# Kernel tuning notes

Hardware: AMD Instinct MI355X
Metric: run time of the kernel (lower is better)

Reference implementation:

```python
import jax, jax.numpy as jnp
import numpy as np

N = 100000
F_IN = 128
E = 1_600_000
NEG_SLOPE = 0.2  # PyG GATConv default negative_slope


def _seg_sum(v, idx, n):
    return jax.ops.segment_sum(v, idx, num_segments=n)


def gcn_conv(x, W, b, src, dst, n):
    # PyG GCNConv: D^{-1/2} (A + I) D^{-1/2} X W + b (self loops already in src/dst)
    h = x @ W
    deg = _seg_sum(jnp.ones(src.shape, h.dtype), dst, n)
    dinv = jnp.where(deg > 0, jax.lax.rsqrt(deg), 0.0)
    norm = dinv[src] * dinv[dst]  # [E]
    return _seg_sum(h[src] * norm[:, None], dst, n) + b


def gat_conv(x, W, a_src, a_dst, b, src, dst, n, heads, out_ch):
    # PyG GATConv (concat=True), eval mode (dropout inactive)
    h = (x @ W).reshape(n, heads, out_ch)          # [n,H,C]
    s = jnp.einsum('nhc,hc->nh', h, a_src)          # per-node src score
    t = jnp.einsum('nhc,hc->nh', h, a_dst)          # per-node dst score
    e = jax.nn.leaky_relu(s[src] + t[dst], NEG_SLOPE)  # [E,H]
    m = jax.ops.segment_max(e, dst, num_segments=n)    # stable segment softmax
    m = jnp.where(jnp.isfinite(m), m, 0.0)
    p = jnp.exp(e - m[dst])
    denom = _seg_sum(p, dst, n)
    alpha = p / (denom[dst] + 1e-16)                 # [E,H]
    out = _seg_sum(h[src] * alpha[:, :, None], dst, n)  # [n,H,C]
    return out.reshape(n, heads * out_ch) + b


def setup_inputs():
    key = jax.random.key(0)
    ks = jax.random.split(key, 24)
    x = jax.random.normal(ks[0], (N, F_IN), jnp.float32) * 0.1
    half = N // 2
    # one-hot user/item type flags read by forward (x[:,0]==1 / x[:,1]==1)
    x = x.at[:, 0].set(0.0).at[:, 1].set(0.0)
    x = x.at[:half, 0].set(1.0).at[half:, 1].set(1.0)
    src = jax.random.randint(ks[1], (E,), 0, N, dtype=jnp.int32)
    dst = jax.random.randint(ks[2], (E,), 0, N, dtype=jnp.int32)
    edge_index = jnp.stack([src, dst])

    def p(k, shape):
        return jax.random.normal(k, shape, jnp.float32) * 0.1

    inp = {"x": x, "edge_index": edge_index,
           "gcn_w": p(ks[3], (F_IN, 16)), "gcn_b": jnp.zeros((16,), jnp.float32)}
    dims = [(16, 16, 8), (128, 16, 8), (128, 16, 8), (128, 2, 1)]
    for i, (fi, fo, h) in enumerate(dims, start=1):
        inp[f"g{i}_w"] = p(ks[3 + 4 * i], (fi, h * fo))
        inp[f"g{i}_as"] = p(ks[4 + 4 * i], (h, fo))
        inp[f"g{i}_ad"] = p(ks[5 + 4 * i], (h, fo))
        inp[f"g{i}_b"] = jnp.zeros((h * fo,), jnp.float32)
    return inp


def reference(x, edge_index, gcn_w, gcn_b,
              g1_w, g1_as, g1_ad, g1_b,
              g2_w, g2_as, g2_ad, g2_b,
              g3_w, g3_as, g3_ad, g3_b,
              g4_w, g4_as, g4_ad, g4_b):
    n = x.shape[0]
    loops = jnp.arange(n, dtype=edge_index.dtype)  # self loops (added by GCN/GAT layers)
    src = jnp.concatenate([edge_index[0], loops])
    dst = jnp.concatenate([edge_index[1], loops])
    h = jax.nn.elu(gcn_conv(x, gcn_w, gcn_b, src, dst, n))
    h = jax.nn.elu(gat_conv(h, g1_w, g1_as, g1_ad, g1_b, src, dst, n, 8, 16))
    h = jax.nn.elu(gat_conv(h, g2_w, g2_as, g2_ad, g2_b, src, dst, n, 8, 16))
    h = jax.nn.elu(gat_conv(h, g3_w, g3_as, g3_ad, g3_b, src, dst, n, 8, 16))
    h = jax.nn.elu(gat_conv(h, g4_w, g4_as, g4_ad, g4_b, src, dst, n, 1, 2))  # [n,2]
    half = n // 2  # users are rows [:half], items rows [half:]
    out = jnp.concatenate([h[:half], h[half:]], axis=1)  # [half,4]
    return jax.nn.log_softmax(out, axis=1)
```

## Files before the change

### kernel.cpp

```cpp
#include <hip/hip_runtime.h>
#include <cstddef>
#include <cstdint>

#define NN 100000
#define NPAD 100032
#define NE 1600000
#define ET (NE + NN)
#define ETP_MAX (ET + 8 * NN)
#define HALFN (NN / 2)
#define NEG_SLOPE 0.2f
#define SCB 1024
#define DMAX 96
#define RP 8
#define RNODES (NN / RP)
#define CHUNK 8192

typedef __attribute__((ext_vector_type(8))) short short8v;
typedef __attribute__((ext_vector_type(4))) float float4v;
typedef __attribute__((ext_vector_type(2))) float float2v;

__device__ __forceinline__ float lrelu(float x) { return x > 0.f ? x : NEG_SLOPE * x; }

__device__ __forceinline__ uint16_t f2bf(float f) {
  uint32_t u = __float_as_uint(f);
  uint32_t r = u + 0x7fffu + ((u >> 16) & 1u);
  return (uint16_t)(r >> 16);
}
__device__ __forceinline__ float bflo(uint32_t u) { return __uint_as_float(u << 16); }
__device__ __forceinline__ float bfhi(uint32_t u) { return __uint_as_float(u & 0xffff0000u); }

template<int K, int M>
__launch_bounds__(256)
__global__ void gemm4_kernel(const float* __restrict__ X, const float* __restrict__ W,
                             float* __restrict__ Y, int n) {
  constexpr int CG = M / 4;
  constexpr int RG = 256 / CG;
  constexpr int RPT = 2;
  constexpr int RT = RG * RPT;
  constexpr int KP = K + 1;
  __shared__ __align__(16) float sW[K * M];
  __shared__ float sX[RT * KP];
  for (int i = threadIdx.x; i < K * M; i += 256) sW[i] = W[i];
  const int jg = threadIdx.x % CG;
  const int rg = threadIdx.x / CG;
  const int r0 = rg * RPT;
  for (int base = blockIdx.x * RT; base < n; base += gridDim.x * RT) {
    __syncthreads();
    const int nrows = (n - base) < RT ? (n - base) : RT;
    for (int i = threadIdx.x; i < nrows * K; i += 256) {
      int r = i / K, c = i - r * K;
      sX[r * KP + c] = X[(size_t)base * K + i];
    }
    __syncthreads();
    float acc[RPT][4];
    #pragma unroll
    for (int rr = 0; rr < RPT; ++rr) acc[rr][0] = acc[rr][1] = acc[rr][2] = acc[rr][3] = 0.f;
    #pragma unroll 4
    for (int k = 0; k < K; ++k) {
      const float4 w = *(const float4*)&sW[k * M + jg * 4];
      #pragma unroll
      for (int rr = 0; rr < RPT; ++rr) {
        const float xv = sX[(r0 + rr) * KP + k];
        acc[rr][0] = fmaf(xv, w.x, acc[rr][0]);
        acc[rr][1] = fmaf(xv, w.y, acc[rr][1]);
        acc[rr][2] = fmaf(xv, w.z, acc[rr][2]);
        acc[rr][3] = fmaf(xv, w.w, acc[rr][3]);
      }
    }
    #pragma unroll
    for (int rr = 0; rr < RPT; ++rr) {
      if (r0 + rr < nrows) {
        float4 o = make_float4(acc[rr][0], acc[rr][1], acc[rr][2], acc[rr][3]);
        *(float4*)&Y[(size_t)(base + r0 + rr) * M + jg * 4] = o;
      }
    }
  }
}

template<int KB>
__launch_bounds__(256)
__global__ void wpack_kernel(const float* __restrict__ W, uint16_t* __restrict__ wp,
                             int Kreal) {
  int tid = blockIdx.x * 256 + threadIdx.x;
  if (tid >= KB * 8 * 64) return;
  int lane = tid & 63;
  int ctkb = tid >> 6;
  int kb = ctkb % KB, ct = ctkb / KB;
  int nc = ct * 16 + (lane & 15);
  int k0 = kb * 32 + (lane >> 4) * 8;
  ushort4 o0, o1;
  uint16_t v[8];
  #pragma unroll
  for (int j = 0; j < 8; ++j) {
    int k = k0 + j;
    v[j] = (k < Kreal) ? f2bf(W[(size_t)k * 128 + nc]) : (uint16_t)0;
  }
  o0.x = v[0]; o0.y = v[1]; o0.z = v[2]; o0.w = v[3];
  o1.x = v[4]; o1.y = v[5]; o1.z = v[6]; o1.w = v[7];
  *(ushort4*)&wp[(size_t)tid * 8] = o0;
  *(ushort4*)&wp[(size_t)tid * 8 + 4] = o1;
}

template<int KB, int XS>
__launch_bounds__(256)
__global__ void gemm_mfma_kernel(const uint16_t* __restrict__ X,
                                 const uint16_t* __restrict__ wp,
                                 uint16_t* __restrict__ Y, int n) {
  __shared__ float sC[4][16 * 136];
  const int wv = threadIdx.x >> 6;
  const int lane = threadIdx.x & 63;
  const int rowbase = blockIdx.x * 64 + wv * 16;
  int arow = rowbase + (lane & 15);
  if (arow >= n) arow = n - 1;
  const uint16_t* xp = X + (size_t)arow * XS + ((lane >> 4) * 8);
  short8v a[KB];
  #pragma unroll
  for (int kb = 0; kb < KB; ++kb) a[kb] = *(const short8v*)(xp + kb * 32);
  #pragma unroll
  for (int ct = 0; ct < 8; ++ct) {
    float4v acc = {0.f, 0.f, 0.f, 0.f};
    #pragma unroll
    for (int kb = 0; kb < KB; ++kb) {
      short8v b = *(const short8v*)&wp[(size_t)((ct * KB + kb) * 64 + lane) * 8];
      acc = __builtin_amdgcn_mfma_f32_16x16x32_bf16(a[kb], b, acc, 0, 0, 0);
    }
    #pragma unroll
    for (int r = 0; r < 4; ++r)
      sC[wv][((lane >> 4) * 4 + r) * 136 + ct * 16 + (lane & 15)] = acc[r];
  }
  #pragma unroll
  for (int t = 0; t < 4; ++t) {
    int idx = t * 64 + lane;
    int row = idx >> 4;
    int c8 = idx & 15;
    const float* pr = &sC[wv][row * 136 + c8 * 8];
    float4 lo = *(const float4*)pr;
    float4 hi = *(const float4*)(pr + 4);
    uint4 o;
    o.x = (uint32_t)f2bf(lo.x) | ((uint32_t)f2bf(lo.y) << 16);
    o.y = (uint32_t)f2bf(lo.z) | ((uint32_t)f2bf(lo.w) << 16);
    o.z = (uint32_t)f2bf(hi.x) | ((uint32_t)f2bf(hi.y) << 16);
    o.w = (uint32_t)f2bf(hi.z) | ((uint32_t)f2bf(hi.w) << 16);
    *(uint4*)&Y[(size_t)(rowbase + row) * 128 + c8 * 8] = o;
  }
}

template<int K, int M, int ROWS>
__launch_bounds__(256)
__global__ void gemm_s_kernel(const uint16_t* __restrict__ Xb, const float* __restrict__ W,
                              float* __restrict__ Y, int n) {
  constexpr int KP = K + 1;
  __shared__ float sW[K * M];
  __shared__ float sX[ROWS * KP];
  for (int i = threadIdx.x; i < K * M; i += 256) sW[i] = W[i];
  for (int base = blockIdx.x * ROWS; base < n; base += gridDim.x * ROWS) {
    __syncthreads();
    const int nrows = (n - base) < ROWS ? (n - base) : ROWS;
    for (int i = threadIdx.x; i < nrows * (K / 4); i += 256) {
      int r = i / (K / 4), c = i - r * (K / 4);
      uint2 u = *(const uint2*)&Xb[(size_t)(base + r) * K + c * 4];
      sX[r * KP + c * 4 + 0] = bflo(u.x);
      sX[r * KP + c * 4 + 1] = bfhi(u.x);
      sX[r * KP + c * 4 + 2] = bflo(u.y);
      sX[r * KP + c * 4 + 3] = bfhi(u.y);
    }
    __syncthreads();
    for (int o = threadIdx.x; o < nrows * M; o += 256) {
      int r = o / M, j = o - r * M;
      float a = 0.f;
      #pragma unroll
      for (int k = 0; k < K; ++k) a = fmaf(sX[r * KP + k], sW[k * M + j], a);
      Y[(size_t)(base + r) * M + j] = a;
    }
  }
}

template<int H, int C>
__launch_bounds__(256)
__global__ void score_bf16_kernel(const uint32_t* __restrict__ Hm,
                                  const float* __restrict__ aS, const float* __restrict__ aD,
                                  float* __restrict__ S, float* __restrict__ T, int n) {
  int idx = blockIdx.x * 256 + threadIdx.x;
  int tot = n * H;
  if (idx >= tot + H) return;
  if (idx >= tot) { S[idx] = -1e30f; T[idx] = 0.f; return; }
  int h = idx & (H - 1);
  const uint32_t* hp = Hm + (size_t)idx * (C / 2);
  float s = 0.f, t = 0.f;
  #pragma unroll
  for (int c2 = 0; c2 < C / 2; ++c2) {
    uint32_t u = hp[c2];
    float v0 = bflo(u), v1 = bfhi(u);
    s = fmaf(v0, aS[h * C + 2 * c2], s);
    s = fmaf(v1, aS[h * C + 2 * c2 + 1], s);
    t = fmaf(v0, aD[h * C + 2 * c2], t);
    t = fmaf(v1, aD[h * C + 2 * c2 + 1], t);
  }
  S[idx] = s;
  T[idx] = t;
}

template<int H, int C>
__launch_bounds__(256)
__global__ void score_kernel(const float* __restrict__ Hm,
                             const float* __restrict__ aS, const float* __restrict__ aD,
                             float* __restrict__ S, float* __restrict__ T, int n) {
  int idx = blockIdx.x * 256 + threadIdx.x;
  int tot = n * H;
  if (idx >= tot + H) return;
  if (idx >= tot) { S[idx] = -1e30f; T[idx] = 0.f; return; }
  int h = idx & (H - 1);
  const float* hp = Hm + (size_t)idx * C;
  float s = 0.f, t = 0.f;
  #pragma unroll
  for (int c = 0; c < C; ++c) {
    float v = hp[c];
    s = fmaf(v, aS[h * C + c], s);
    t = fmaf(v, aD[h * C + c], t);
  }
  S[idx] = s;
  T[idx] = t;
}

__launch_bounds__(256)
__global__ void rank_kernel(const int* __restrict__ edst, int* __restrict__ cursor,
                            int* __restrict__ rank) {
  int e = blockIdx.x * 256 + threadIdx.x;
  if (e >= ET) return;
  int dn = e < NE ? edst[e] : e - NE;
  rank[e] = atomicAdd(&cursor[dn], 1);
}

__device__ __forceinline__ int pad8(int d) { return (d + 7) & ~7; }

__launch_bounds__(256)
__global__ void scan1_kernel(const int* __restrict__ degi, int* __restrict__ rowptr,
                             int* __restrict__ bsums) {
  __shared__ int sd[256];
  int t = threadIdx.x;
  int base = blockIdx.x * SCB + t * 4;
  int v0 = base + 0 < NN ? pad8(degi[base + 0]) : 0;
  int v1 = base + 1 < NN ? pad8(degi[base + 1]) : 0;
  int v2 = base + 2 < NN ? pad8(degi[base + 2]) : 0;
  int v3 = base + 3 < NN ? pad8(degi[base + 3]) : 0;
  int s = v0 + v1 + v2 + v3;
  sd[t] = s;
  __syncthreads();
  for (int off = 1; off < 256; off <<= 1) {
    int x = (t >= off) ? sd[t - off] : 0;
    __syncthreads();
    sd[t] += x;
    __syncthreads();
  }
  int excl = sd[t] - s;
  if (t == 255) bsums[blockIdx.x] = sd[255];
  if (base + 0 < NN) rowptr[base + 0] = excl;
  excl += v0;
  if (base + 1 < NN) rowptr[base + 1] = excl;
  excl += v1;
  if (base + 2 < NN) rowptr[base + 2] = excl;
  excl += v2;
  if (base + 3 < NN) rowptr[base + 3] = excl;
}

__launch_bounds__(256)
__global__ void scan2_kernel(int* __restrict__ bsums, int nb) {
  __shared__ int sd[256];
  int t = threadIdx.x;
  int v = t < nb ? bsums[t] : 0;
  sd[t] = v;
  __syncthreads();
  for (int off = 1; off < 256; off <<= 1) {
    int x = (t >= off) ? sd[t - off] : 0;
    __syncthreads();
    sd[t] += x;
    __syncthreads();
  }
  if (t < nb) bsums[t] = sd[t] - v;
  if (t == nb - 1) bsums[nb] = sd[t];
}

__launch_bounds__(256)
__global__ void scan3_kernel(int* __restrict__ rowptr, const int* __restrict__ bsums, int nb) {
  int i = blockIdx.x * 256 + threadIdx.x;
  if (i < NN) rowptr[i] += bsums[i / SCB];
  if (i == 0) rowptr[NN] = bsums[nb];
}

__launch_bounds__(256)
__global__ void dinv_kernel(const int* __restrict__ deg, float* __restrict__ dinv) {
  int i = blockIdx.x * 256 + threadIdx.x;
  if (i > NN) return;
  if (i == NN) { dinv[i] = 0.f; return; }
  int d = deg[i];
  dinv[i] = d > 0 ? rsqrtf((float)d) : 0.f;
}

__launch_bounds__(256)
__global__ void csr_fill_kernel(int* __restrict__ csr) {
  int i = blockIdx.x * 256 + threadIdx.x;
  if (i < ETP_MAX) csr[i] = NN;
}

__launch_bounds__(256)
__global__ void scatter_part_kernel(const int* __restrict__ esrc, const int* __restrict__ edst,
                                    const int* __restrict__ rowptr, const int* __restrict__ rank,
                                    int* __restrict__ csr_src) {
  int p = blockIdx.x & (RP - 1);
  int c = blockIdx.x >> 3;
  int lo = p * RNODES, hi = lo + RNODES;
  int e0 = c * CHUNK;
  int e1 = e0 + CHUNK < ET ? e0 + CHUNK : ET;
  for (int e = e0 + threadIdx.x; e < e1; e += 256) {
    int dn = e < NE ? edst[e] : e - NE;
    if (dn >= lo && dn < hi) {
      int sn = e < NE ? esrc[e] : e - NE;
      csr_src[rowptr[dn] + rank[e]] = sn;
    }
  }
}

__launch_bounds__(256)
__global__ void fused_gat_kernel(const int* __restrict__ rowptr, const int* __restrict__ csr,
                                 const float* __restrict__ S, const float* __restrict__ T,
                                 const uint16_t* __restrict__ Hm, const float* __restrict__ bias,
                                 float* __restrict__ galpha, uint16_t* __restrict__ Outb) {
  __shared__ float lds_p[4][DMAX * 9];
  __shared__ int   lds_c[4][DMAX];
  const int wv = threadIdx.x >> 6;
  const int lane = threadIdx.x & 63;
  const int d = (blockIdx.x * 256 + threadIdx.x) >> 6;
  if (d >= NN) return;
  const int rs = rowptr[d];
  const int deg = rowptr[d + 1] - rs;
  const int degL = deg < DMAX ? deg : DMAX;
  const char* sb = (const char*)S;
  const char* hb = (const char*)Hm;
  const int h = lane & 7, g = lane >> 3;
  const float Th = T[(size_t)d * 8 + h];
  float m = -1e30f;
  for (int l = g; l < degL; l += 8) {
    int sn = csr[rs + l];
    float sv = *(const float*)(sb + (((uint32_t)sn << 5) + (h << 2)));
    float e = lrelu(sv + Th);
    lds_p[wv][l * 9 + h] = e;
    if (h == 0) lds_c[wv][l] = sn;
    m = fmaxf(m, e);
  }
  for (int l = DMAX + g; l < deg; l += 8) {
    int sn = csr[rs + l];
    float e = lrelu(*(const float*)(sb + (((uint32_t)sn << 5) + (h << 2))) + Th);
    galpha[(size_t)(rs + l) * 8 + h] = e;
    m = fmaxf(m, e);
  }
  #pragma unroll
  for (int mask = 8; mask < 64; mask <<= 1) m = fmaxf(m, __shfl_xor(m, mask));
  float sum = 0.f;
  for (int l = g; l < degL; l += 8) {
    float p = __expf(lds_p[wv][l * 9 + h] - m);
    lds_p[wv][l * 9 + h] = p;
    sum += p;
  }
  for (int l = DMAX + g; l < deg; l += 8) {
    float p = __expf(galpha[(size_t)(rs + l) * 8 + h] - m);
    galpha[(size_t)(rs + l) * 8 + h] = p;
    sum += p;
  }
  #pragma unroll
  for (int mask = 8; mask < 64; mask <<= 1) sum += __shfl_xor(sum, mask);
  const float inv = 1.f / (sum + 1e-16f);
  const int eg = lane >> 4;
  const int cl = lane & 15;
  const int hp = cl >> 1;
  const float invp = __shfl(inv, hp);
  float2v A0 = {0.f, 0.f}, A1 = {0.f, 0.f}, A2 = {0.f, 0.f}, A3 = {0.f, 0.f};
  const uint32_t clo = (uint32_t)(cl << 4);
  #pragma unroll 2
  for (int l0 = 0; l0 < degL; l0 += 4) {
    int lc = l0 + eg;
    int sn = lds_c[wv][lc];
    float p = lds_p[wv][lc * 9 + hp];
    float2v pp = {p, p};
    uint4 u = *(const uint4*)(hb + (((uint32_t)sn << 8) + clo));
    float2v h0 = {bflo(u.x), bfhi(u.x)};
    float2v h1 = {bflo(u.y), bfhi(u.y)};
    float2v h2 = {bflo(u.z), bfhi(u.z)};
    float2v h3 = {bflo(u.w), bfhi(u.w)};
    A0 = pp * h0 + A0;
    A1 = pp * h1 + A1;
    A2 = pp * h2 + A2;
    A3 = pp * h3 + A3;
  }
  for (int l0 = DMAX; l0 < deg; l0 += 4) {
    int lc = l0 + eg;
    int sn = csr[rs + lc];
    float p = galpha[(size_t)(rs + lc) * 8 + hp];
    float2v pp = {p, p};
    uint4 u = *(const uint4*)(hb + (((uint32_t)sn << 8) + clo));
    float2v h0 = {bflo(u.x), bfhi(u.x)};
    float2v h1 = {bflo(u.y), bfhi(u.y)};
    float2v h2 = {bflo(u.z), bfhi(u.z)};
    float2v h3 = {bflo(u.w), bfhi(u.w)};
    A0 = pp * h0 + A0;
    A1 = pp * h1 + A1;
    A2 = pp * h2 + A2;
    A3 = pp * h3 + A3;
  }
  #pragma unroll
  for (int mask = 16; mask < 64; mask <<= 1) {
    A0.x += __shfl_xor(A0.x, mask); A0.y += __shfl_xor(A0.y, mask);
    A1.x += __shfl_xor(A1.x, mask); A1.y += __shfl_xor(A1.y, mask);
    A2.x += __shfl_xor(A2.x, mask); A2.y += __shfl_xor(A2.y, mask);
    A3.x += __shfl_xor(A3.x, mask); A3.y += __shfl_xor(A3.y, mask);
  }
  if (lane < 16) {
    float4 b0 = *(const float4*)&bias[cl * 8];
    float4 b1 = *(const float4*)&bias[cl * 8 + 4];
    float v0 = fmaf(A0.x, invp, b0.x), v1 = fmaf(A0.y, invp, b0.y);
    float v2 = fmaf(A1.x, invp, b0.z), v3 = fmaf(A1.y, invp, b0.w);
    float v4 = fmaf(A2.x, invp, b1.x), v5 = fmaf(A2.y, invp, b1.y);
    float v6 = fmaf(A3.x, invp, b1.z), v7 = fmaf(A3.y, invp, b1.w);
    v0 = v0 > 0.f ? v0 : expm1f(v0); v1 = v1 > 0.f ? v1 : expm1f(v1);
    v2 = v2 > 0.f ? v2 : expm1f(v2); v3 = v3 > 0.f ? v3 : expm1f(v3);
    v4 = v4 > 0.f ? v4 : expm1f(v4); v5 = v5 > 0.f ? v5 : expm1f(v5);
    v6 = v6 > 0.f ? v6 : expm1f(v6); v7 = v7 > 0.f ? v7 : expm1f(v7);
    uint4 o;
    o.x = (uint32_t)f2bf(v0) | ((uint32_t)f2bf(v1) << 16);
    o.y = (uint32_t)f2bf(v2) | ((uint32_t)f2bf(v3) << 16);
    o.z = (uint32_t)f2bf(v4) | ((uint32_t)f2bf(v5) << 16);
    o.w = (uint32_t)f2bf(v6) | ((uint32_t)f2bf(v7) << 16);
    *(uint4*)&Outb[(size_t)d * 128 + cl * 8] = o;
  }
}

__launch_bounds__(256)
__global__ void fused_gat1_kernel(const int* __restrict__ rowptr, const int* __restrict__ csr,
                                  const float* __restrict__ S, const float* __restrict__ T,
                                  const float* __restrict__ Hm2, const float* __restrict__ bias,
                                  float* __restrict__ galpha, float* __restrict__ Out) {
  int d = (blockIdx.x * 256 + threadIdx.x) >> 6;
  if (d >= NN) return;
  int lane = threadIdx.x & 63;
  int rs = rowptr[d], deg = rowptr[d + 1] - rs;
  float Td = T[d];
  int sn = 0;
  float e = -1e30f;
  if (lane < deg) { sn = csr[rs + lane]; e = lrelu(S[sn] + Td); }
  float m = e;
  for (int l2 = 64 + lane; l2 < deg; l2 += 64) {
    float e2 = lrelu(S[csr[rs + l2]] + Td);
    galpha[rs + l2] = e2;
    m = fmaxf(m, e2);
  }
  #pragma unroll
  for (int mask = 1; mask < 64; mask <<= 1) m = fmaxf(m, __shfl_xor(m, mask));
  float p = (lane < deg) ? __expf(e - m) : 0.f;
  float sum = p;
  for (int l2 = 64 + lane; l2 < deg; l2 += 64) {
    float p2 = __expf(galpha[rs + l2] - m);
    galpha[rs + l2] = p2;
    sum += p2;
  }
  #pragma unroll
  for (int mask = 1; mask < 64; mask <<= 1) sum += __shfl_xor(sum, mask);
  float inv = 1.f / (sum + 1e-16f);
  float a0 = 0.f, a1 = 0.f;
  if (lane < deg) {
    float2 hv = *(const float2*)&Hm2[(size_t)sn * 2];
    a0 = p * hv.x; a1 = p * hv.y;
  }
  for (int l2 = 64 + lane; l2 < deg; l2 += 64) {
    int sn2 = csr[rs + l2];
    float p2 = galpha[rs + l2];
    float2 hv = *(const float2*)&Hm2[(size_t)sn2 * 2];
    a0 = fmaf(p2, hv.x, a0); a1 = fmaf(p2, hv.y, a1);
  }
  #pragma unroll
  for (int mask = 1; mask < 64; mask <<= 1) {
    a0 += __shfl_xor(a0, mask); a1 += __shfl_xor(a1, mask);
  }
  if (lane == 0) {
    float v0 = fmaf(a0, inv, bias[0]);
    float v1 = fmaf(a1, inv, bias[1]);
    v0 = v0 > 0.f ? v0 : expm1f(v0);
    v1 = v1 > 0.f ? v1 : expm1f(v1);
    float2 o; o.x = v0; o.y = v1;
    *(float2*)&Out[(size_t)d * 2] = o;
  }
}

__launch_bounds__(256)
__global__ void gcn_pull_kernel(const int* __restrict__ rowptr, const int* __restrict__ csr_src,
                                const float* __restrict__ dinv, const float* __restrict__ Hm,
                                const float* __restrict__ bias, uint16_t* __restrict__ Outb) {
  int d = blockIdx.x * 16 + threadIdx.x / 16;
  if (d >= NN) return;
  int f = threadIdx.x & 15;
  int rs = rowptr[d], re = rowptr[d + 1];
  float acc = 0.f;
  int j = rs;
  for (; j + 4 <= re; j += 4) {
    int s0 = csr_src[j], s1 = csr_src[j + 1], s2 = csr_src[j + 2], s3 = csr_src[j + 3];
    float d0 = dinv[s0], d1 = dinv[s1], d2 = dinv[s2], d3 = dinv[s3];
    float h0 = Hm[(size_t)s0 * 16 + f], h1 = Hm[(size_t)s1 * 16 + f];
    float h2 = Hm[(size_t)s2 * 16 + f], h3 = Hm[(size_t)s3 * 16 + f];
    acc = fmaf(d0, h0, acc); acc = fmaf(d1, h1, acc);
    acc = fmaf(d2, h2, acc); acc = fmaf(d3, h3, acc);
  }
  for (; j < re; ++j) {
    int sn = csr_src[j];
    acc = fmaf(dinv[sn], Hm[(size_t)sn * 16 + f], acc);
  }
  float v = acc * dinv[d] + bias[f];
  v = v > 0.f ? v : expm1f(v);
  Outb[(size_t)d * 32 + f] = f2bf(v);
  Outb[(size_t)d * 32 + 16 + f] = 0;
}

__launch_bounds__(256)
__global__ void final_kernel(const float* __restrict__ A, float* __restrict__ Out) {
  int i = blockIdx.x * 256 + threadIdx.x;
  if (i >= HALFN) return;
  float v0 = A[(size_t)i * 2 + 0];
  float v1 = A[(size_t)i * 2 + 1];
  float v2 = A[(size_t)(i + HALFN) * 2 + 0];
  float v3 = A[(size_t)(i + HALFN) * 2 + 1];
  float m = fmaxf(fmaxf(v0, v1), fmaxf(v2, v3));
  float e0 = __expf(v0 - m), e1 = __expf(v1 - m), e2 = __expf(v2 - m), e3 = __expf(v3 - m);
  float l = logf(e0 + e1 + e2 + e3) + m;
  Out[(size_t)i * 4 + 0] = v0 - l;
  Out[(size_t)i * 4 + 1] = v1 - l;
  Out[(size_t)i * 4 + 2] = v2 - l;
  Out[(size_t)i * 4 + 3] = v3 - l;
}

extern "C" void kernel_launch(void* const* d_in, const int* in_sizes, int n_in,
                              void* d_out, int out_size, void* d_ws, size_t ws_size,
                              hipStream_t stream) {
  const float* x     = (const float*)d_in[0];
  const int*   eidx  = (const int*)d_in[1];
  const int*   esrc  = eidx;
  const int*   edst  = eidx + NE;
  const float* gcn_w = (const float*)d_in[2];
  const float* gcn_b = (const float*)d_in[3];

  char* ws = (char*)d_ws;
  uint16_t* hbf    = (uint16_t*)(ws + 0);
  uint16_t* bufAb  = (uint16_t*)(ws + 25700000);
  uint16_t* gcnHbf = (uint16_t*)(ws + 51400000);
  float*    bufB   = (float*)   (ws + 57900000);
  float*    bufC   = (float*)   (ws + 64400000);
  float*    Sb     = (float*)   (ws + 65300000);
  float*    Tb     = (float*)   (ws + 68600000);
  float*    galpha = (float*)   (ws + 71900000);
  int*      rowptr = (int*)     (ws + 151900000);
  int*      cursor = (int*)     (ws + 152300008);
  int*      csr    = (int*)     (ws + 152700008);
  float*    dinv   = (float*)   (ws + 162700008);
  int*      bsums  = (int*)     (ws + 163100016);
  int*      rank   = (int*)     (ws + 163100528);
  uint16_t* wpck   = (uint16_t*)(ws + 169900528);

  constexpr int NB_SCAN = (NN + SCB - 1) / SCB;

  hipMemsetAsync(cursor, 0, (size_t)NN * 4, stream);
  rank_kernel<<<(ET + 255) / 256, 256, 0, stream>>>(edst, cursor, rank);
  scan1_kernel<<<NB_SCAN, 256, 0, stream>>>(cursor, rowptr, bsums);
  scan2_kernel<<<1, 256, 0, stream>>>(bsums, NB_SCAN);
  scan3_kernel<<<(NN + 256) / 256, 256, 0, stream>>>(rowptr, bsums, NB_SCAN);
  dinv_kernel<<<(NN + 256) / 256, 256, 0, stream>>>(cursor, dinv);
  csr_fill_kernel<<<(ETP_MAX + 255) / 256, 256, 0, stream>>>(csr);
  {
    int nch = (ET + CHUNK - 1) / CHUNK;
    scatter_part_kernel<<<nch * RP, 256, 0, stream>>>(esrc, edst, rowptr, rank, csr);
  }

  {
    int tiles = (NN + 127) / 128;
    if (tiles > 4096) tiles = 4096;
    gemm4_kernel<128, 16><<<tiles, 256, 0, stream>>>(x, gcn_w, bufB, NN);
  }
  gcn_pull_kernel<<<(NN + 15) / 16, 256, 0, stream>>>(rowptr, csr, dinv, bufB, gcn_b, gcnHbf);

  wpack_kernel<1><<<2, 256, 0, stream>>>((const float*)d_in[4], wpck, 16);
  gemm_mfma_kernel<1, 32><<<NPAD / 64, 256, 0, stream>>>(gcnHbf, wpck, hbf, NN);
  score_bf16_kernel<8, 16><<<(NN * 8 + 8 + 255) / 256, 256, 0, stream>>>(
      (const uint32_t*)hbf, (const float*)d_in[5], (const float*)d_in[6], Sb, Tb, NN);
  fused_gat_kernel<<<(NN * 64 + 255) / 256, 256, 0, stream>>>(
      rowptr, csr, Sb, Tb, hbf, (const float*)d_in[7], galpha, bufAb);

  wpack_kernel<4><<<8, 256, 0, stream>>>((const float*)d_in[8], wpck, 128);
  gemm_mfma_kernel<4, 128><<<NPAD / 64, 256, 0, stream>>>(bufAb, wpck, hbf, NN);
  score_bf16_kernel<8, 16><<<(NN * 8 + 8 + 255) / 256, 256, 0, stream>>>(
      (const uint32_t*)hbf, (const float*)d_in[9], (const float*)d_in[10], Sb, Tb, NN);
  fused_gat_kernel<<<(NN * 64 + 255) / 256, 256, 0, stream>>>(
      rowptr, csr, Sb, Tb, hbf, (const float*)d_in[11], galpha, bufAb);

  wpack_kernel<4><<<8, 256, 0, stream>>>((const float*)d_in[12], wpck, 128);
  gemm_mfma_kernel<4, 128><<<NPAD / 64, 256, 0, stream>>>(bufAb, wpck, hbf, NN);
  score_bf16_kernel<8, 16><<<(NN * 8 + 8 + 255) / 256, 256, 0, stream>>>(
      (const uint32_t*)hbf, (const float*)d_in[13], (const float*)d_in[14], Sb, Tb, NN);
  fused_gat_kernel<<<(NN * 64 + 255) / 256, 256, 0, stream>>>(
      rowptr, csr, Sb, Tb, hbf, (const float*)d_in[15], galpha, bufAb);

  {
    int tiles = (NN + 127) / 128;
    if (tiles > 2048) tiles = 2048;
    gemm_s_kernel<128, 2, 128><<<tiles, 256, 0, stream>>>(
        bufAb, (const float*)d_in[16], bufB, NN);
    score_kernel<1, 2><<<(NN + 1 + 255) / 256, 256, 0, stream>>>(
        bufB, (const float*)d_in[17], (const float*)d_in[18], Sb, Tb, NN);
    fused_gat1_kernel<<<(NN * 64 + 255) / 256, 256, 0, stream>>>(
        rowptr, csr, Sb, Tb, bufB, (const float*)d_in[19], galpha, bufC);
  }

  final_kernel<<<(HALFN + 255) / 256, 256, 0, stream>>>(bufC, (float*)d_out);
}
```

Before: 585.4 us.

## Use single-pass online softmax in GAT aggregation and pad CSR rows to 4

The three-pass GAT aggregation (max pass, exp/sum pass, weighted sum pass, with LDS staging and a global spill for high-degree nodes) becomes one pass using an online softmax. Each lane group keeps a running max, sum and rescaled accumulators, and the groups are merged with xor shuffles at the end. CSR row padding drops from 8 to 4 to match the 4-edge step of the loop, which cuts padded edges. This removes LDS use, the galpha buffer and the repeated csr/S reads, at the cost of extra exp calls and occasional rescaling branches per edge.

```diff
diff --git a/kernel.cpp b/kernel.cpp
--- a/kernel.cpp
+++ b/kernel.cpp
@@ -6,11 +6,10 @@
 #define NPAD 100032
 #define NE 1600000
 #define ET (NE + NN)
-#define ETP_MAX (ET + 8 * NN)
+#define ETP_MAX (ET + 4 * NN)
 #define HALFN (NN / 2)
 #define NEG_SLOPE 0.2f
 #define SCB 1024
-#define DMAX 96
 #define RP 8
 #define RNODES (NN / RP)
 #define CHUNK 8192
@@ -231,7 +230,7 @@
   rank[e] = atomicAdd(&cursor[dn], 1);
 }
 
-__device__ __forceinline__ int pad8(int d) { return (d + 7) & ~7; }
+__device__ __forceinline__ int pad4(int d) { return (d + 3) & ~3; }
 
 __launch_bounds__(256)
 __global__ void scan1_kernel(const int* __restrict__ degi, int* __restrict__ rowptr,
@@ -239,10 +238,10 @@
   __shared__ int sd[256];
   int t = threadIdx.x;
   int base = blockIdx.x * SCB + t * 4;
-  int v0 = base + 0 < NN ? pad8(degi[base + 0]) : 0;
-  int v1 = base + 1 < NN ? pad8(degi[base + 1]) : 0;
-  int v2 = base + 2 < NN ? pad8(degi[base + 2]) : 0;
-  int v3 = base + 3 < NN ? pad8(degi[base + 3]) : 0;
+  int v0 = base + 0 < NN ? pad4(degi[base + 0]) : 0;
+  int v1 = base + 1 < NN ? pad4(degi[base + 1]) : 0;
+  int v2 = base + 2 < NN ? pad4(degi[base + 2]) : 0;
+  int v3 = base + 3 < NN ? pad4(degi[base + 3]) : 0;
   int s = v0 + v1 + v2 + v3;
   sd[t] = s;
   __syncthreads();
@@ -324,102 +323,70 @@
 __global__ void fused_gat_kernel(const int* __restrict__ rowptr, const int* __restrict__ csr,
                                  const float* __restrict__ S, const float* __restrict__ T,
                                  const uint16_t* __restrict__ Hm, const float* __restrict__ bias,
-                                 float* __restrict__ galpha, uint16_t* __restrict__ Outb) {
-  __shared__ float lds_p[4][DMAX * 9];
-  __shared__ int   lds_c[4][DMAX];
-  const int wv = threadIdx.x >> 6;
+                                 uint16_t* __restrict__ Outb) {
   const int lane = threadIdx.x & 63;
   const int d = (blockIdx.x * 256 + threadIdx.x) >> 6;
   if (d >= NN) return;
   const int rs = rowptr[d];
   const int deg = rowptr[d + 1] - rs;
-  const int degL = deg < DMAX ? deg : DMAX;
-  const char* sb = (const char*)S;
-  const char* hb = (const char*)Hm;
-  const int h = lane & 7, g = lane >> 3;
-  const float Th = T[(size_t)d * 8 + h];
-  float m = -1e30f;
-  for (int l = g; l < degL; l += 8) {
-    int sn = csr[rs + l];
-    float sv = *(const float*)(sb + (((uint32_t)sn << 5) + (h << 2)));
-    float e = lrelu(sv + Th);
-    lds_p[wv][l * 9 + h] = e;
-    if (h == 0) lds_c[wv][l] = sn;
-    m = fmaxf(m, e);
-  }
-  for (int l = DMAX + g; l < deg; l += 8) {
-    int sn = csr[rs + l];
-    float e = lrelu(*(const float*)(sb + (((uint32_t)sn << 5) + (h << 2))) + Th);
-    galpha[(size_t)(rs + l) * 8 + h] = e;
-    m = fmaxf(m, e);
-  }
-  #pragma unroll
-  for (int mask = 8; mask < 64; mask <<= 1) m = fmaxf(m, __shfl_xor(m, mask));
-  float sum = 0.f;
-  for (int l = g; l < degL; l += 8) {
-    float p = __expf(lds_p[wv][l * 9 + h] - m);
-    lds_p[wv][l * 9 + h] = p;
-    sum += p;
-  }
-  for (int l = DMAX + g; l < deg; l += 8) {
-    float p = __expf(galpha[(size_t)(rs + l) * 8 + h] - m);
-    galpha[(size_t)(rs + l) * 8 + h] = p;
-    sum += p;
-  }
-  #pragma unroll
-  for (int mask = 8; mask < 64; mask <<= 1) sum += __shfl_xor(sum, mask);
-  const float inv = 1.f / (sum + 1e-16f);
   const int eg = lane >> 4;
   const int cl = lane & 15;
   const int hp = cl >> 1;
-  const float invp = __shfl(inv, hp);
+  const float Th = T[(size_t)d * 8 + hp];
+  const char* sb = (const char*)S;
+  const char* hb = (const char*)Hm;
+  float m = -1e38f;
+  float s = 0.f;
   float2v A0 = {0.f, 0.f}, A1 = {0.f, 0.f}, A2 = {0.f, 0.f}, A3 = {0.f, 0.f};
   const uint32_t clo = (uint32_t)(cl << 4);
-  #pragma unroll 2
-  for (int l0 = 0; l0 < degL; l0 += 4) {
-    int lc = l0 + eg;
-    int sn = lds_c[wv][lc];
-    float p = lds_p[wv][lc * 9 + hp];
-    float2v pp = {p, p};
-    uint4 u = *(const uint4*)(hb + (((uint32_t)sn << 8) + clo));
-    float2v h0 = {bflo(u.x), bfhi(u.x)};
-    float2v h1 = {bflo(u.y), bfhi(u.y)};
-    float2v h2 = {bflo(u.z), bfhi(u.z)};
-    float2v h3 = {bflo(u.w), bfhi(u.w)};
-    A0 = pp * h0 + A0;
-    A1 = pp * h1 + A1;
-    A2 = pp * h2 + A2;
-    A3 = pp * h3 + A3;
-  }
-  for (int l0 = DMAX; l0 < deg; l0 += 4) {
+  const uint32_t hpo = (uint32_t)(hp << 2);
+  for (int l0 = 0; l0 < deg; l0 += 4) {
     int lc = l0 + eg;
     int sn = csr[rs + lc];
-    float p = galpha[(size_t)(rs + lc) * 8 + hp];
+    uint4 u = *(const uint4*)(hb + (((uint32_t)sn << 8) + clo));
+    float sv = *(const float*)(sb + (((uint32_t)sn << 5) + hpo));
+    float e = lrelu(sv + Th);
+    float nm = fmaxf(m, e);
+    float p = __expf(e - nm);
+    if (e > m) {
+      float sc = __expf(m - nm);
+      float2v scv = {sc, sc};
+      s *= sc;
+      A0 *= scv; A1 *= scv; A2 *= scv; A3 *= scv;
+      m = nm;
+    }
+    s += p;
     float2v pp = {p, p};
-    uint4 u = *(const uint4*)(hb + (((uint32_t)sn << 8) + clo));
-    float2v h0 = {bflo(u.x), bfhi(u.x)};
-    float2v h1 = {bflo(u.y), bfhi(u.y)};
-    float2v h2 = {bflo(u.z), bfhi(u.z)};
-    float2v h3 = {bflo(u.w), bfhi(u.w)};
-    A0 = pp * h0 + A0;
-    A1 = pp * h1 + A1;
-    A2 = pp * h2 + A2;
-    A3 = pp * h3 + A3;
-  }
-  #pragma unroll
-  for (int mask = 16; mask < 64; mask <<= 1) {
-    A0.x += __shfl_xor(A0.x, mask); A0.y += __shfl_xor(A0.y, mask);
-    A1.x += __shfl_xor(A1.x, mask); A1.y += __shfl_xor(A1.y, mask);
-    A2.x += __shfl_xor(A2.x, mask); A2.y += __shfl_xor(A2.y, mask);
-    A3.x += __shfl_xor(A3.x, mask); A3.y += __shfl_xor(A3.y, mask);
+    A0 = pp * (float2v){bflo(u.x), bfhi(u.x)} + A0;
+    A1 = pp * (float2v){bflo(u.y), bfhi(u.y)} + A1;
+    A2 = pp * (float2v){bflo(u.z), bfhi(u.z)} + A2;
+    A3 = pp * (float2v){bflo(u.w), bfhi(u.w)} + A3;
+  }
+  #pragma unroll
+  for (int mask = 16; mask <= 32; mask <<= 1) {
+    float om = __shfl_xor(m, mask);
+    float os = __shfl_xor(s, mask);
+    float o0x = __shfl_xor(A0.x, mask), o0y = __shfl_xor(A0.y, mask);
+    float o1x = __shfl_xor(A1.x, mask), o1y = __shfl_xor(A1.y, mask);
+    float o2x = __shfl_xor(A2.x, mask), o2y = __shfl_xor(A2.y, mask);
+    float o3x = __shfl_xor(A3.x, mask), o3y = __shfl_xor(A3.y, mask);
+    float nm = fmaxf(m, om);
+    float s1 = __expf(m - nm), s2 = __expf(om - nm);
+    s = s * s1 + os * s2;
+    A0.x = A0.x * s1 + o0x * s2; A0.y = A0.y * s1 + o0y * s2;
+    A1.x = A1.x * s1 + o1x * s2; A1.y = A1.y * s1 + o1y * s2;
+    A2.x = A2.x * s1 + o2x * s2; A2.y = A2.y * s1 + o2y * s2;
+    A3.x = A3.x * s1 + o3x * s2; A3.y = A3.y * s1 + o3y * s2;
+    m = nm;
   }
   if (lane < 16) {
+    const float inv = 1.f / (s + 1e-16f);
     float4 b0 = *(const float4*)&bias[cl * 8];
     float4 b1 = *(const float4*)&bias[cl * 8 + 4];
-    float v0 = fmaf(A0.x, invp, b0.x), v1 = fmaf(A0.y, invp, b0.y);
-    float v2 = fmaf(A1.x, invp, b0.z), v3 = fmaf(A1.y, invp, b0.w);
-    float v4 = fmaf(A2.x, invp, b1.x), v5 = fmaf(A2.y, invp, b1.y);
-    float v6 = fmaf(A3.x, invp, b1.z), v7 = fmaf(A3.y, invp, b1.w);
+    float v0 = fmaf(A0.x, inv, b0.x), v1 = fmaf(A0.y, inv, b0.y);
+    float v2 = fmaf(A1.x, inv, b0.z), v3 = fmaf(A1.y, inv, b0.w);
+    float v4 = fmaf(A2.x, inv, b1.x), v5 = fmaf(A2.y, inv, b1.y);
+    float v6 = fmaf(A3.x, inv, b1.z), v7 = fmaf(A3.y, inv, b1.w);
     v0 = v0 > 0.f ? v0 : expm1f(v0); v1 = v1 > 0.f ? v1 : expm1f(v1);
     v2 = v2 > 0.f ? v2 : expm1f(v2); v3 = v3 > 0.f ? v3 : expm1f(v3);
     v4 = v4 > 0.f ? v4 : expm1f(v4); v5 = v5 > 0.f ? v5 : expm1f(v5);
@@ -587,21 +554,21 @@
   score_bf16_kernel<8, 16><<<(NN * 8 + 8 + 255) / 256, 256, 0, stream>>>(
       (const uint32_t*)hbf, (const float*)d_in[5], (const float*)d_in[6], Sb, Tb, NN);
   fused_gat_kernel<<<(NN * 64 + 255) / 256, 256, 0, stream>>>(
-      rowptr, csr, Sb, Tb, hbf, (const float*)d_in[7], galpha, bufAb);
+      rowptr, csr, Sb, Tb, hbf, (const float*)d_in[7], bufAb);
 
   wpack_kernel<4><<<8, 256, 0, stream>>>((const float*)d_in[8], wpck, 128);
   gemm_mfma_kernel<4, 128><<<NPAD / 64, 256, 0, stream>>>(bufAb, wpck, hbf, NN);
   score_bf16_kernel<8, 16><<<(NN * 8 + 8 + 255) / 256, 256, 0, stream>>>(
       (const uint32_t*)hbf, (const float*)d_in[9], (const float*)d_in[10], Sb, Tb, NN);
   fused_gat_kernel<<<(NN * 64 + 255) / 256, 256, 0, stream>>>(
-      rowptr, csr, Sb, Tb, hbf, (const float*)d_in[11], galpha, bufAb);
+      rowptr, csr, Sb, Tb, hbf, (const float*)d_in[11], bufAb);
 
   wpack_kernel<4><<<8, 256, 0, stream>>>((const float*)d_in[12], wpck, 128);
   gemm_mfma_kernel<4, 128><<<NPAD / 64, 256, 0, stream>>>(bufAb, wpck, hbf, NN);
   score_bf16_kernel<8, 16><<<(NN * 8 + 8 + 255) / 256, 256, 0, stream>>>(
       (const uint32_t*)hbf, (const float*)d_in[13], (const float*)d_in[14], Sb, Tb, NN);
   fused_gat_kernel<<<(NN * 64 + 255) / 256, 256, 0, stream>>>(
-      rowptr, csr, Sb, Tb, hbf, (const float*)d_in[15], galpha, bufAb);
+      rowptr, csr, Sb, Tb, hbf, (const float*)d_in[15], bufAb);
 
   {
     int tiles = (NN + 127) / 128;
```

After: 588.7 us. No clear change (+0.6%).
